# Optimization experiments

Measured on AMD Instinct MI355X. Metric: run time of the kernel, lower is better.

## Reference

```python
import jax, jax.numpy as jnp
import numpy as np

B, H, D = 32, 168, 512
HIST, FORE, NF = 336, 168, 8


def setup_inputs() -> dict:
    key = jax.random.key(0)
    ks = jax.random.split(key, 11)
    inp = {
        "y_hat": jax.random.normal(ks[0], (B, H, D), dtype=jnp.float32),
        "weather_hist": jax.random.normal(ks[1], (B, HIST, NF), dtype=jnp.float32),
        "weather_fore": jax.random.normal(ks[2], (B, FORE, NF), dtype=jnp.float32),
        # query_proj: Linear(D, D)
        "Wq": jax.random.normal(ks[3], (D, D), dtype=jnp.float32) * 0.02,
        "bq": jax.random.normal(ks[4], (D,), dtype=jnp.float32) * 0.02,
        # key_proj / value_proj: Linear(1, D) -> weight is a single column [D]
        "Wk": jax.random.normal(ks[5], (D,), dtype=jnp.float32) * 0.02,
        "bk": jax.random.normal(ks[6], (D,), dtype=jnp.float32) * 0.02,
        "Wv": jax.random.normal(ks[7], (D,), dtype=jnp.float32) * 0.02,
        "bv": jax.random.normal(ks[8], (D,), dtype=jnp.float32) * 0.02,
        # score_proj: Linear(D, D)
        "Ws": jax.random.normal(ks[9], (D, D), dtype=jnp.float32) * 0.02,
        "bs": jax.random.normal(ks[10], (D,), dtype=jnp.float32) * 0.02,
    }
    return inp


def reference(y_hat, weather_hist, weather_fore, Wq, bq, Wk, bk, Wv, bv, Ws, bs):
    # y_hat: [B,H,D]; weather_*: [B,T,F]
    scale = jnp.asarray(y_hat.shape[-1], jnp.float32) ** 0.5
    full = jnp.concatenate([weather_hist, weather_fore], axis=1)  # [B,L,F]
    n_factors = full.shape[-1]

    Q = y_hat @ Wq.T + bq  # [B,H,D]

    # key_proj(feature) = feature * Wk + bk (Linear with in_features=1), so
    # Q @ K^T factors exactly: attn[b,f,h,l] = (Q@Wk)[b,h]*full[b,l,f] + (Q@bk)[b,h]
    qk = Q @ Wk  # [B,H]
    qb = Q @ bk  # [B,H]
    attn = (qk[:, None, :, None] * jnp.transpose(full, (0, 2, 1))[:, :, None, :]
            + qb[:, None, :, None]) / scale  # [B,F,H,L]
    weight = jax.nn.softmax(attn, axis=-1)  # softmax over L

    # V = full*Wv + bv; corr = weight @ V. Rows of weight sum to 1, so the bv
    # term contributes exactly bv per feature -> n_factors*bv after the sum over f.
    s = jnp.einsum('bfhl,blf->bfh', weight, full)  # [B,F,H]
    correction = jnp.einsum('bfh,d->bhd', s, Wv) + n_factors * bv  # [B,H,D]

    combined = correction @ Ws.T + bs  # [B,H,D]
    logits = jnp.sum(combined * y_hat, axis=-1, keepdims=True) / scale  # [B,H,1]
    P = jax.nn.softmax(logits, axis=1)  # softmax over horizon H
    final = jnp.sum(P * y_hat, axis=1, keepdims=True)  # [B,1,D]
    return y_hat + final  # broadcast of final.expand_as(y_hat)
```

## Files before the change

### kernel.cpp

```cpp
#include <hip/hip_runtime.h>
#include <math.h>

#define NB 32
#define NH 168
#define ND 512
#define NHIST 336
#define NFORE 168
#define NL 504
#define NF 8
#define LOG2E 1.4426950408889634f
#define SCALE 22.627416997969522f

__device__ inline float waveSum(float v) {
    #pragma unroll
    for (int m = 1; m < 64; m <<= 1) v += __shfl_xor(v, m, 64);
    return v;
}
__device__ inline float grpSum32(float v) {
    v += __shfl_xor(v, 1, 64);
    v += __shfl_xor(v, 2, 64);
    v += __shfl_xor(v, 4, 64);
    v += __shfl_xor(v, 8, 64);
    v += __shfl_xor(v, 16, 64);
    return v;
}

__global__ __launch_bounds__(256) void k_pre(
        const float* __restrict__ Wq, const float* __restrict__ bq,
        const float* __restrict__ Wk, const float* __restrict__ Wv,
        const float* __restrict__ bv, const float* __restrict__ Ws,
        const float* __restrict__ bs,
        float* __restrict__ uk2, float* __restrict__ wvs2,
        float* __restrict__ bvs2, float* __restrict__ ckp) {
    const int blk = blockIdx.x, tid = threadIdx.x;
    __shared__ float red[256];
    if (blk < 32) {
        const int c = tid & 15, rg = tid >> 4;
        const int colbase = blk << 4;
        float acc = 0.f;
        #pragma unroll
        for (int r = 0; r < 32; ++r) {
            const int e = rg + 16 * r;
            acc += Wk[e] * Wq[e * ND + colbase + c];
        }
        red[rg * 16 + c] = acc;
        __syncthreads();
        if (tid < 16) {
            float s = 0.f;
            #pragma unroll
            for (int i = 0; i < 16; ++i) s += red[i * 16 + tid];
            uk2[colbase + tid] = s * (LOG2E / SCALE);
        }
    } else if (blk < 96) {
        const int g = tid >> 5, sl = tid & 31;
        const int e = ((blk - 32) << 3) + g;
        const float4* __restrict__ wsr = (const float4*)(Ws + (size_t)e * ND);
        const float4* __restrict__ wv4 = (const float4*)Wv;
        const float4* __restrict__ bv4 = (const float4*)bv;
        float a1 = 0.f, a2 = 0.f;
        #pragma unroll
        for (int i = 0; i < 4; ++i) {
            const int q = sl + 32 * i;
            const float4 x = wsr[q];
            const float4 v = wv4[q];
            const float4 c = bv4[q];
            a1 += x.x * v.x + x.y * v.y + x.z * v.z + x.w * v.w;
            a2 += x.x * c.x + x.y * c.y + x.z * c.z + x.w * c.w;
        }
        a1 = grpSum32(a1);
        a2 = grpSum32(a2);
        if (sl == 0) {
            wvs2[e] = a1 * (1.f / SCALE);
            bvs2[e] = (8.f * a2 + bs[e]) * (1.f / SCALE);
        }
    } else {
        const int lane = tid & 63, w = tid >> 6;
        float p = bq[tid] * Wk[tid] + bq[tid + 256] * Wk[tid + 256];
        p = waveSum(p);
        if (lane == 0) red[w] = p;
        __syncthreads();
        if (tid == 0)
            *ckp = (red[0] + red[1] + red[2] + red[3]) * (LOG2E / SCALE);
    }
}

__global__ __launch_bounds__(256) void k_main(
        const float* __restrict__ y, const float* __restrict__ wh,
        const float* __restrict__ wf,
        const float* __restrict__ uk2, const float* __restrict__ wvs2,
        const float* __restrict__ bvs2, const float* __restrict__ ckp,
        float* __restrict__ logits) {
    const int blk = blockIdx.x, tid = threadIdx.x;
    const int b = blk / 21, hb = blk % 21;
    const int slot = tid >> 5, sl = tid & 31;
    const int h = hb * 8 + slot;

    const float4* __restrict__ yr  = (const float4*)(y + ((size_t)b * NH + h) * ND);
    const float4* __restrict__ uk4 = (const float4*)uk2;
    const float4* __restrict__ wv4 = (const float4*)wvs2;
    const float4* __restrict__ bv4 = (const float4*)bvs2;
    float d1 = 0.f, d2 = 0.f, d3 = 0.f;
    #pragma unroll
    for (int i = 0; i < 4; ++i) {
        const int q = sl + 32 * i;
        const float4 yv = yr[q];
        const float4 u = uk4[q];
        const float4 v = wv4[q];
        const float4 c = bv4[q];
        d1 += yv.x * u.x + yv.y * u.y + yv.z * u.z + yv.w * u.w;
        d2 += yv.x * v.x + yv.y * v.y + yv.z * v.z + yv.w * v.w;
        d3 += yv.x * c.x + yv.y * c.y + yv.z * c.z + yv.w * c.w;
    }
    d1 = grpSum32(d1); d2 = grpSum32(d2); d3 = grpSum32(d3);
    const float a2 = d1 + *ckp;

    const float4* __restrict__ whp = (const float4*)(wh + (size_t)b * NHIST * NF);
    const float4* __restrict__ wfp = (const float4*)(wf + (size_t)b * NFORE * NF);
    float numf[NF], denf[NF];
    #pragma unroll
    for (int f = 0; f < NF; ++f) { numf[f] = 0.f; denf[f] = 0.f; }
    #pragma unroll
    for (int i = 0; i < 16; ++i) {
        const int l = sl + 32 * i;
        if (l < NL) {
            const float4* __restrict__ src =
                (l < NHIST) ? (whp + (size_t)l * 2) : (wfp + (size_t)(l - NHIST) * 2);
            const float4 xa = src[0];
            const float4 xb = src[1];
            const float e0 = __builtin_amdgcn_exp2f(a2 * xa.x);
            const float e1 = __builtin_amdgcn_exp2f(a2 * xa.y);
            const float e2 = __builtin_amdgcn_exp2f(a2 * xa.z);
            const float e3 = __builtin_amdgcn_exp2f(a2 * xa.w);
            const float e4 = __builtin_amdgcn_exp2f(a2 * xb.x);
            const float e5 = __builtin_amdgcn_exp2f(a2 * xb.y);
            const float e6 = __builtin_amdgcn_exp2f(a2 * xb.z);
            const float e7 = __builtin_amdgcn_exp2f(a2 * xb.w);
            numf[0] += xa.x * e0; denf[0] += e0;
            numf[1] += xa.y * e1; denf[1] += e1;
            numf[2] += xa.z * e2; denf[2] += e2;
            numf[3] += xa.w * e3; denf[3] += e3;
            numf[4] += xb.x * e4; denf[4] += e4;
            numf[5] += xb.y * e5; denf[5] += e5;
            numf[6] += xb.z * e6; denf[6] += e6;
            numf[7] += xb.w * e7; denf[7] += e7;
        }
    }
    #pragma unroll
    for (int m = 1; m < 32; m <<= 1) {
        #pragma unroll
        for (int f = 0; f < NF; ++f) {
            numf[f] += __shfl_xor(numf[f], m, 64);
            denf[f] += __shfl_xor(denf[f], m, 64);
        }
    }
    float S = 0.f;
    #pragma unroll
    for (int f = 0; f < NF; ++f)
        S += numf[f] * __builtin_amdgcn_rcpf(denf[f]);
    if (sl == 0) logits[b * NH + h] = S * d2 + d3;
}

__global__ __launch_bounds__(256) void k_final(
        const float* __restrict__ y, const float* __restrict__ logits,
        float* __restrict__ out) {
    const int b = blockIdx.x >> 4, dc = blockIdx.x & 15;
    const int tid = threadIdx.x, lane = tid & 63, w = tid >> 6;
    __shared__ float el[NH];
    __shared__ float invz;
    __shared__ float4 fl4[32];
    __shared__ float4 ffin[8];
    if (tid < NH)
        el[tid] = __builtin_amdgcn_exp2f(logits[b * NH + tid] * LOG2E);
    __syncthreads();
    if (w == 0) {
        float z = 0.f;
        for (int i = lane; i < NH; i += 64) z += el[i];
        z = waveSum(z);
        if (lane == 0) invz = 1.f / z;
    }
    __syncthreads();

    const int c = tid & 7, hw = tid >> 3;
    const float4* __restrict__ y4 = (const float4*)y;
    const size_t base = ((size_t)b * NH) * 128 + dc * 8 + c;
    float4 acc = make_float4(0.f, 0.f, 0.f, 0.f);
    #pragma unroll
    for (int k = 0; k < 6; ++k) {
        const int hh = hw + 32 * k;
        if (hh < NH) {
            const float4 yv = y4[base + (size_t)hh * 128];
            const float P = el[hh];
            acc.x += P * yv.x; acc.y += P * yv.y;
            acc.z += P * yv.z; acc.w += P * yv.w;
        }
    }
    #pragma unroll
    for (int m = 8; m < 64; m <<= 1) {
        acc.x += __shfl_xor(acc.x, m, 64);
        acc.y += __shfl_xor(acc.y, m, 64);
        acc.z += __shfl_xor(acc.z, m, 64);
        acc.w += __shfl_xor(acc.w, m, 64);
    }
    if (lane < 8) fl4[w * 8 + lane] = acc;
    __syncthreads();
    if (tid < 8) {
        float4 s = fl4[tid];
        #pragma unroll
        for (int i = 1; i < 4; ++i) {
            const float4 t = fl4[i * 8 + tid];
            s.x += t.x; s.y += t.y; s.z += t.z; s.w += t.w;
        }
        const float iz = invz;
        s.x *= iz; s.y *= iz; s.z *= iz; s.w *= iz;
        ffin[tid] = s;
    }
    __syncthreads();
    const float4 fin = ffin[c];
    float4* __restrict__ out4 = (float4*)out;
    #pragma unroll
    for (int k = 0; k < 6; ++k) {
        const int hh = hw + 32 * k;
        if (hh < NH) {
            float4 o = y4[base + (size_t)hh * 128];
            o.x += fin.x; o.y += fin.y; o.z += fin.z; o.w += fin.w;
            out4[base + (size_t)hh * 128] = o;
        }
    }
}

extern "C" void kernel_launch(void* const* d_in, const int* in_sizes, int n_in,
                              void* d_out, int out_size, void* d_ws, size_t ws_size,
                              hipStream_t stream) {
    const float* y  = (const float*)d_in[0];
    const float* wh = (const float*)d_in[1];
    const float* wf = (const float*)d_in[2];
    const float* Wq = (const float*)d_in[3];
    const float* bq = (const float*)d_in[4];
    const float* Wk = (const float*)d_in[5];
    const float* Wv = (const float*)d_in[7];
    const float* bv = (const float*)d_in[8];
    const float* Ws = (const float*)d_in[9];
    const float* bs = (const float*)d_in[10];
    float* out = (float*)d_out;
    float* ws = (float*)d_ws;

    float* uk2  = ws;
    float* wvs2 = ws + 512;
    float* bvs2 = ws + 1024;
    float* ckp  = ws + 1536;
    float* logits = ws + 2048;

    k_pre<<<97, 256, 0, stream>>>(Wq, bq, Wk, Wv, bv, Ws, bs,
                                  uk2, wvs2, bvs2, ckp);
    k_main<<<NB * 21, 256, 0, stream>>>(y, wh, wf, uk2, wvs2, bvs2, ckp, logits);
    k_final<<<NB * 16, 256, 0, stream>>>(y, logits, out);
}
```

Baseline: 24.28 us.

## Fuse weight-precompute and main kernels using a global atomic flag handoff

Merges the weight-precompute kernel into the main logits kernel. The first 97 blocks compute the precomputed vectors and signal completion by incrementing a device-scope atomic counter, and the remaining blocks prefetch their y rows into registers before spinning on that counter. This is meant to remove one kernel launch boundary and overlap the y loads with the precompute. It adds a memset launch, relies on the producer blocks being scheduled before or alongside the consumers to avoid deadlock, and sets launch bounds for occupancy.

```diff
diff --git a/kernel.cpp b/kernel.cpp
--- a/kernel.cpp
+++ b/kernel.cpp
@@ -10,6 +10,7 @@
 #define NF 8
 #define LOG2E 1.4426950408889634f
 #define SCALE 22.627416997969522f
+#define NPRE 97
 
 __device__ inline float waveSum(float v) {
     #pragma unroll
@@ -25,91 +26,121 @@
     return v;
 }
 
-__global__ __launch_bounds__(256) void k_pre(
+__global__ __launch_bounds__(256, 4) void k_mega(
+        const float* __restrict__ y, const float* __restrict__ wh,
+        const float* __restrict__ wf,
         const float* __restrict__ Wq, const float* __restrict__ bq,
         const float* __restrict__ Wk, const float* __restrict__ Wv,
         const float* __restrict__ bv, const float* __restrict__ Ws,
         const float* __restrict__ bs,
         float* __restrict__ uk2, float* __restrict__ wvs2,
-        float* __restrict__ bvs2, float* __restrict__ ckp) {
+        float* __restrict__ bvs2, float* __restrict__ ckp,
+        float* __restrict__ logits, unsigned* __restrict__ flag) {
     const int blk = blockIdx.x, tid = threadIdx.x;
-    __shared__ float red[256];
-    if (blk < 32) {
-        const int c = tid & 15, rg = tid >> 4;
-        const int colbase = blk << 4;
-        float acc = 0.f;
-        #pragma unroll
-        for (int r = 0; r < 32; ++r) {
-            const int e = rg + 16 * r;
-            acc += Wk[e] * Wq[e * ND + colbase + c];
-        }
-        red[rg * 16 + c] = acc;
-        __syncthreads();
-        if (tid < 16) {
-            float s = 0.f;
+
+    if (blk < NPRE) {
+        __shared__ float red[256];
+        if (blk < 32) {
+            const int c = tid & 15, rg = tid >> 4;
+            const int colbase = blk << 4;
+            float acc = 0.f;
             #pragma unroll
-            for (int i = 0; i < 16; ++i) s += red[i * 16 + tid];
-            uk2[colbase + tid] = s * (LOG2E / SCALE);
-        }
-    } else if (blk < 96) {
-        const int g = tid >> 5, sl = tid & 31;
-        const int e = ((blk - 32) << 3) + g;
-        const float4* __restrict__ wsr = (const float4*)(Ws + (size_t)e * ND);
-        const float4* __restrict__ wv4 = (const float4*)Wv;
-        const float4* __restrict__ bv4 = (const float4*)bv;
-        float a1 = 0.f, a2 = 0.f;
-        #pragma unroll
-        for (int i = 0; i < 4; ++i) {
-            const int q = sl + 32 * i;
-            const float4 x = wsr[q];
-            const float4 v = wv4[q];
-            const float4 c = bv4[q];
-            a1 += x.x * v.x + x.y * v.y + x.z * v.z + x.w * v.w;
-            a2 += x.x * c.x + x.y * c.y + x.z * c.z + x.w * c.w;
-        }
-        a1 = grpSum32(a1);
-        a2 = grpSum32(a2);
-        if (sl == 0) {
-            wvs2[e] = a1 * (1.f / SCALE);
-            bvs2[e] = (8.f * a2 + bs[e]) * (1.f / SCALE);
-        }
-    } else {
-        const int lane = tid & 63, w = tid >> 6;
-        float p = bq[tid] * Wk[tid] + bq[tid + 256] * Wk[tid + 256];
-        p = waveSum(p);
-        if (lane == 0) red[w] = p;
+            for (int r = 0; r < 32; ++r) {
+                const int e = rg + 16 * r;
+                acc += Wk[e] * Wq[e * ND + colbase + c];
+            }
+            red[rg * 16 + c] = acc;
+            __syncthreads();
+            if (tid < 16) {
+                float s = 0.f;
+                #pragma unroll
+                for (int i = 0; i < 16; ++i) s += red[i * 16 + tid];
+                uk2[colbase + tid] = s * (LOG2E / SCALE);
+            }
+        } else if (blk < 96) {
+            const int g = tid >> 5, sl = tid & 31;
+            const int e = ((blk - 32) << 3) + g;
+            const float4* __restrict__ wsr = (const float4*)(Ws + (size_t)e * ND);
+            const float4* __restrict__ wv4 = (const float4*)Wv;
+            const float4* __restrict__ bv4 = (const float4*)bv;
+            float a1 = 0.f, a2 = 0.f;
+            #pragma unroll
+            for (int i = 0; i < 4; ++i) {
+                const int q = sl + 32 * i;
+                const float4 x = wsr[q];
+                const float4 v = wv4[q];
+                const float4 c = bv4[q];
+                a1 += x.x * v.x + x.y * v.y + x.z * v.z + x.w * v.w;
+                a2 += x.x * c.x + x.y * c.y + x.z * c.z + x.w * c.w;
+            }
+            a1 = grpSum32(a1);
+            a2 = grpSum32(a2);
+            if (sl == 0) {
+                wvs2[e] = a1 * (1.f / SCALE);
+                bvs2[e] = (8.f * a2 + bs[e]) * (1.f / SCALE);
+            }
+        } else {
+            const int lane = tid & 63, w = tid >> 6;
+            float p = bq[tid] * Wk[tid] + bq[tid + 256] * Wk[tid + 256];
+            p = waveSum(p);
+            if (lane == 0) red[w] = p;
+            __syncthreads();
+            if (tid == 0)
+                *ckp = (red[0] + red[1] + red[2] + red[3]) * (LOG2E / SCALE);
+        }
         __syncthreads();
         if (tid == 0)
-            *ckp = (red[0] + red[1] + red[2] + red[3]) * (LOG2E / SCALE);
-    }
-}
-
-__global__ __launch_bounds__(256) void k_main(
-        const float* __restrict__ y, const float* __restrict__ wh,
-        const float* __restrict__ wf,
-        const float* __restrict__ uk2, const float* __restrict__ wvs2,
-        const float* __restrict__ bvs2, const float* __restrict__ ckp,
-        float* __restrict__ logits) {
-    const int blk = blockIdx.x, tid = threadIdx.x;
-    const int b = blk / 21, hb = blk % 21;
+            __hip_atomic_fetch_add(flag, 1u, __ATOMIC_RELEASE,
+                                   __HIP_MEMORY_SCOPE_AGENT);
+        return;
+    }
+
+    const int cblk = blk - NPRE;
+    const int b = cblk / 21, hb = cblk % 21;
     const int slot = tid >> 5, sl = tid & 31;
     const int h = hb * 8 + slot;
 
-    const float4* __restrict__ yr  = (const float4*)(y + ((size_t)b * NH + h) * ND);
+    const float4* __restrict__ yr = (const float4*)(y + ((size_t)b * NH + h) * ND);
+    float4 yv0 = yr[sl];
+    float4 yv1 = yr[sl + 32];
+    float4 yv2 = yr[sl + 64];
+    float4 yv3 = yr[sl + 96];
+    asm volatile("" :: "v"(yv0.x), "v"(yv0.y), "v"(yv0.z), "v"(yv0.w));
+    asm volatile("" :: "v"(yv1.x), "v"(yv1.y), "v"(yv1.z), "v"(yv1.w));
+    asm volatile("" :: "v"(yv2.x), "v"(yv2.y), "v"(yv2.z), "v"(yv2.w));
+    asm volatile("" :: "v"(yv3.x), "v"(yv3.y), "v"(yv3.z), "v"(yv3.w));
+
+    if (tid == 0) {
+        while (__hip_atomic_load(flag, __ATOMIC_RELAXED,
+                                 __HIP_MEMORY_SCOPE_AGENT) < (unsigned)NPRE)
+            __builtin_amdgcn_s_sleep(8);
+        (void)__hip_atomic_load(flag, __ATOMIC_ACQUIRE,
+                                __HIP_MEMORY_SCOPE_AGENT);
+    }
+    __syncthreads();
+
     const float4* __restrict__ uk4 = (const float4*)uk2;
     const float4* __restrict__ wv4 = (const float4*)wvs2;
     const float4* __restrict__ bv4 = (const float4*)bvs2;
     float d1 = 0.f, d2 = 0.f, d3 = 0.f;
-    #pragma unroll
-    for (int i = 0; i < 4; ++i) {
-        const int q = sl + 32 * i;
-        const float4 yv = yr[q];
-        const float4 u = uk4[q];
-        const float4 v = wv4[q];
-        const float4 c = bv4[q];
-        d1 += yv.x * u.x + yv.y * u.y + yv.z * u.z + yv.w * u.w;
-        d2 += yv.x * v.x + yv.y * v.y + yv.z * v.z + yv.w * v.w;
-        d3 += yv.x * c.x + yv.y * c.y + yv.z * c.z + yv.w * c.w;
+    {
+        float4 u, v, c;
+        u = uk4[sl];      v = wv4[sl];      c = bv4[sl];
+        d1 += yv0.x*u.x + yv0.y*u.y + yv0.z*u.z + yv0.w*u.w;
+        d2 += yv0.x*v.x + yv0.y*v.y + yv0.z*v.z + yv0.w*v.w;
+        d3 += yv0.x*c.x + yv0.y*c.y + yv0.z*c.z + yv0.w*c.w;
+        u = uk4[sl+32];   v = wv4[sl+32];   c = bv4[sl+32];
+        d1 += yv1.x*u.x + yv1.y*u.y + yv1.z*u.z + yv1.w*u.w;
+        d2 += yv1.x*v.x + yv1.y*v.y + yv1.z*v.z + yv1.w*v.w;
+        d3 += yv1.x*c.x + yv1.y*c.y + yv1.z*c.z + yv1.w*c.w;
+        u = uk4[sl+64];   v = wv4[sl+64];   c = bv4[sl+64];
+        d1 += yv2.x*u.x + yv2.y*u.y + yv2.z*u.z + yv2.w*u.w;
+        d2 += yv2.x*v.x + yv2.y*v.y + yv2.z*v.z + yv2.w*v.w;
+        d3 += yv2.x*c.x + yv2.y*c.y + yv2.z*c.z + yv2.w*c.w;
+        u = uk4[sl+96];   v = wv4[sl+96];   c = bv4[sl+96];
+        d1 += yv3.x*u.x + yv3.y*u.y + yv3.z*u.z + yv3.w*u.w;
+        d2 += yv3.x*v.x + yv3.y*v.y + yv3.z*v.z + yv3.w*v.w;
+        d3 += yv3.x*c.x + yv3.y*c.y + yv3.z*c.z + yv3.w*c.w;
     }
     d1 = grpSum32(d1); d2 = grpSum32(d2); d3 = grpSum32(d3);
     const float a2 = d1 + *ckp;
@@ -244,14 +275,16 @@
     float* out = (float*)d_out;
     float* ws = (float*)d_ws;
 
-    float* uk2  = ws;
-    float* wvs2 = ws + 512;
-    float* bvs2 = ws + 1024;
-    float* ckp  = ws + 1536;
-    float* logits = ws + 2048;
-
-    k_pre<<<97, 256, 0, stream>>>(Wq, bq, Wk, Wv, bv, Ws, bs,
-                                  uk2, wvs2, bvs2, ckp);
-    k_main<<<NB * 21, 256, 0, stream>>>(y, wh, wf, uk2, wvs2, bvs2, ckp, logits);
+    float*    uk2    = ws;
+    float*    wvs2   = ws + 512;
+    float*    bvs2   = ws + 1024;
+    float*    ckp    = ws + 1536;
+    float*    logits = ws + 2048;
+    unsigned* flag   = (unsigned*)(ws + 8192);
+
+    hipMemsetAsync(flag, 0, sizeof(unsigned), stream);
+    k_mega<<<NPRE + NB * 21, 256, 0, stream>>>(y, wh, wf, Wq, bq, Wk, Wv, bv,
+                                               Ws, bs, uk2, wvs2, bvs2, ckp,
+                                               logits, flag);
     k_final<<<NB * 16, 256, 0, stream>>>(y, logits, out);
 }
```

Result: slower. 38.93 us (+60.4%).
